# Kernel optimization log

Measured on AMD Instinct MI355X. Metric: run time of the kernel, lower is better.

## Reference

```python
import jax, jax.numpy as jnp
import numpy as np

N = 100000      # hits
K = 256         # max truth objects per event
C = 2           # n_ccoords
NCLS = 6        # n_classes
Q_MIN = 0.5
S_B = 1.0
ENERGY_DEN_OFFSET = 1.0
PAYLOAD_BETA_CLIP = 0.1
USE_AVG_CC = 0.0
BETA_CLIP = 1.0 - 1e-5


def _divide_no_nan(num, den):
    return jnp.where(den == 0.0, 0.0, num / jnp.where(den == 0.0, 1.0, den))


def setup_inputs() -> dict:
    key = jax.random.key(0)
    ks = jax.random.split(key, 12)
    pred_beta = jax.random.uniform(ks[0], (N, 1), minval=0.01, maxval=0.99)
    pred_ccoords = jax.random.normal(ks[1], (N, C))
    pred_energy = jax.random.uniform(ks[2], (N, 1), minval=0.0, maxval=100.0)
    pred_pos = 50.0 * jax.random.normal(ks[3], (N, 2))
    pred_time = jax.random.normal(ks[4], (N, 1))
    pred_id = jax.random.normal(ks[5], (N, NCLS))
    t_energy = jax.random.uniform(ks[6], (N, 1), minval=0.1, maxval=100.0)
    t_pos = 50.0 * jax.random.normal(ks[7], (N, 2))
    t_time = jax.random.normal(ks[8], (N, 1))
    t_pid = jax.random.randint(ks[9], (N, 1), 1, NCLS + 1).astype(jnp.float32)
    t_idx = jax.random.randint(ks[10], (N, 1), -1, K)  # -1 == noise
    rowsplits = jnp.array([0, N], dtype=jnp.int32)
    return dict(pred_beta=pred_beta, pred_ccoords=pred_ccoords,
                pred_energy=pred_energy, pred_pos=pred_pos,
                pred_time=pred_time, pred_id=pred_id,
                t_energy=t_energy, t_pos=t_pos, t_time=t_time, t_pid=t_pid,
                t_idx=t_idx, rowsplits=rowsplits)


def oc_loss(pred_beta, pred_ccoords, pred_energy, pred_pos, pred_time,
            pred_id, t_energy, t_pos, t_time, t_pid, t_idx):
    beta = jnp.clip(pred_beta[:, 0], 0.0, BETA_CLIP)          # [N]
    q = jnp.arctanh(beta) ** 2 + Q_MIN                        # [N] charge
    tidx = t_idx[:, 0]
    not_noise = tidx >= 0                                     # [N]
    tclip = jnp.where(not_noise, tidx, 0)

    # hit->object assignment matrix [N, K]
    M = jax.nn.one_hot(tclip, K, dtype=beta.dtype) * not_noise[:, None].astype(beta.dtype)
    counts = M.sum(axis=0)                                    # [K]
    obj_valid = counts > 0.0
    n_valid = jnp.maximum(obj_valid.sum().astype(beta.dtype), 1.0)

    # condensation point per object: highest-beta hit of that object
    score = jnp.where(M > 0.0, beta[:, None], -1.0)           # [N, K]
    alpha = jnp.argmax(score, axis=0)                         # [K]
    x_alpha = pred_ccoords[alpha]                             # [K, C]
    mean_cc = (M.T @ pred_ccoords) / jnp.maximum(counts, 1.0)[:, None]
    x_k = USE_AVG_CC * mean_cc + (1.0 - USE_AVG_CC) * x_alpha
    q_alpha = q[alpha]                                        # [K]
    beta_alpha = beta[alpha]

    # pairwise hit <-> condensation-point squared distances [N, K]
    diff = pred_ccoords[:, None, :] - x_k[None, :, :]
    distsq = jnp.sum(diff * diff, axis=-1)

    qq = q[:, None] * q_alpha[None, :]                        # [N, K]
    # attractive potential: own-object hits pulled toward condensation point
    v_att_k = (M * distsq * qq).sum(axis=0) / jnp.maximum(counts, 1.0)
    V_att = jnp.where(obj_valid, v_att_k, 0.0).sum() / n_valid
    # repulsive potential: all other hits pushed out of a unit ball
    hinge = jax.nn.relu(1.0 - jnp.sqrt(distsq + 1e-6))
    v_rep_k = ((1.0 - M) * hinge * qq).sum(axis=0) / jnp.maximum(N - counts, 1.0)
    V_rep = jnp.where(obj_valid, v_rep_k, 0.0).sum() / n_valid

    # beta terms: sharpen condensation points, suppress noise beta
    L_beta = jnp.where(obj_valid, 1.0 - beta_alpha, 0.0).sum() / n_valid
    n_noise = jnp.maximum((~not_noise).astype(beta.dtype).sum(), 1.0)
    L_noise = S_B * jnp.where(not_noise, 0.0, beta).sum() / n_noise

    # --- per-hit payload losses ---
    ew = jax.nn.relu(jnp.where(t_energy > 10.0,
                               1.0, (t_energy - 0.5) / 10.0 * 10.0 / 9.5))
    e_loss = _divide_no_nan((t_energy - pred_energy) ** 2,
                            t_energy + ENERGY_DEN_OFFSET)
    p_loss = jnp.sum((t_pos - pred_pos) ** 2, axis=-1, keepdims=True) / 100.0
    tm_loss = (t_time - pred_time) ** 2
    cls_loss = 1e-8 * jnp.mean(pred_id ** 2, axis=-1, keepdims=True)
    payload = jnp.concatenate([e_loss, p_loss, tm_loss, cls_loss], axis=-1) * ew  # [N,4]
    payload = jnp.where(pred_beta < PAYLOAD_BETA_CLIP, 0.0, payload)

    # beta-weighted average of payload over each truth object
    pw = beta * not_noise.astype(beta.dtype)                  # [N]
    num = M.T @ (payload * pw[:, None])                       # [K, 4]
    den = (M * pw[:, None]).sum(axis=0)                       # [K]
    per_obj = num / jnp.maximum(den, 1e-6)[:, None]
    L_payload = (jnp.where(obj_valid[:, None], per_obj, 0.0).sum(axis=0) / n_valid).sum()

    return V_att + V_rep + L_beta + L_noise + L_payload


def reference(pred_beta, pred_ccoords, pred_energy, pred_pos, pred_time,
              pred_id, t_energy, t_pos, t_time, t_pid, t_idx, rowsplits):
    return oc_loss(pred_beta, pred_ccoords, pred_energy, pred_pos, pred_time,
                   pred_id, t_energy, t_pos, t_time, t_pid, t_idx)
```

## Files before the change

kernel.cpp:

```cpp
#include <hip/hip_runtime.h>
#include <hip/hip_bf16.h>
#include <math.h>

#define KOBJ 256
#define B1   256
#define NBH  391
#define HSTR 392
#define QMIN 0.5f
#define BETA_CLIP_C (1.0f - 1e-5f)

typedef unsigned long long u64;

__global__ __launch_bounds__(256) void partials(
    const float*  __restrict__ pred_beta,
    const float*  __restrict__ pred_energy,
    const float2* __restrict__ pred_pos,
    const float*  __restrict__ pred_time,
    const float2* __restrict__ pred_id2,
    const float*  __restrict__ t_energy,
    const float2* __restrict__ t_pos,
    const float*  __restrict__ t_time,
    const int*    __restrict__ t_idx,
    u64*    __restrict__ pk_part,
    float*  __restrict__ cnt_part,
    float*  __restrict__ den_part,
    float4* __restrict__ num_part,
    float*  __restrict__ noise_part,
    int n)
{
    __shared__ u64   spk[KOBJ];
    __shared__ float scnt[KOBJ];
    __shared__ float sden[KOBJ], sn0[KOBJ], sn1[KOBJ], sn2[KOBJ], sn3[KOBJ];
    __shared__ float snoise[256];
    int t = threadIdx.x;
    int b = blockIdx.x;
    spk[t] = 0; scnt[t] = 0.f; sden[t] = 0.f;
    sn0[t] = 0.f; sn1[t] = 0.f; sn2[t] = 0.f; sn3[t] = 0.f;
    __syncthreads();

    float noise = 0.0f;
    for (int i = b * 256 + t; i < n; i += B1 * 256) {
        int tid = t_idx[i];
        float braw = pred_beta[i];
        float beta = fminf(fmaxf(braw, 0.0f), BETA_CLIP_C);
        if (tid >= 0) {
            atomicAdd(&scnt[tid], 1.0f);
            u64 key = ((u64)__float_as_uint(beta) << 32) |
                      (u64)(0x7FFFFFFFu - (unsigned)i);
            atomicMax(&spk[tid], key);
            float te = t_energy[i];
            float ew = (te > 10.0f) ? 1.0f : fmaxf(0.0f, (te - 0.5f) / 9.5f);
            float de = te - pred_energy[i];
            float el = de * de / (te + 1.0f);
            float2 tp = t_pos[i];
            float2 pp = pred_pos[i];
            float dpx = tp.x - pp.x, dpy = tp.y - pp.y;
            float pl = (dpx * dpx + dpy * dpy) * 0.01f;
            float dt = t_time[i] - pred_time[i];
            float tl = dt * dt;
            float2 id0 = pred_id2[3 * i];
            float2 id1 = pred_id2[3 * i + 1];
            float2 id2 = pred_id2[3 * i + 2];
            float cs = id0.x * id0.x + id0.y * id0.y + id1.x * id1.x +
                       id1.y * id1.y + id2.x * id2.x + id2.y * id2.y;
            cs *= (1e-8f / 6.0f);
            float mask = (braw < 0.1f) ? 0.0f : 1.0f;
            float w = mask * ew * beta;
            atomicAdd(&sden[tid], beta);
            atomicAdd(&sn0[tid], el * w);
            atomicAdd(&sn1[tid], pl * w);
            atomicAdd(&sn2[tid], tl * w);
            atomicAdd(&sn3[tid], cs * w);
        } else {
            noise += beta;
        }
    }
    __syncthreads();
    int o = t * B1 + b;
    pk_part[o]  = spk[t];
    cnt_part[o] = scnt[t];
    den_part[o] = sden[t];
    num_part[o] = make_float4(sn0[t], sn1[t], sn2[t], sn3[t]);
    snoise[t] = noise;
    __syncthreads();
    for (int s = 128; s > 0; s >>= 1) {
        if (t < s) snoise[t] += snoise[t + s];
        __syncthreads();
    }
    if (t == 0) noise_part[b] = snoise[0];
}

__global__ __launch_bounds__(256) void merge(
    const float2* __restrict__ pred_ccoords,
    const u64*    __restrict__ pk_part,
    const float*  __restrict__ cnt_part,
    const float*  __restrict__ den_part,
    const float4* __restrict__ num_part,
    float4* __restrict__ objA,
    float4* __restrict__ objB)
{
    __shared__ u64   spk[256];
    __shared__ float scnt[256], sden[256], snum[256];
    int k = blockIdx.x;
    int b = threadIdx.x;
    int o = k * B1 + b;
    u64 pk = pk_part[o];
    float cnt = cnt_part[o];
    float den = den_part[o];
    float4 v = num_part[o];
    float nsum = v.x + v.y + v.z + v.w;
    spk[b] = pk; scnt[b] = cnt; sden[b] = den; snum[b] = nsum;
    __syncthreads();
    for (int s = 128; s > 0; s >>= 1) {
        if (b < s) {
            u64 p = spk[b + s]; if (p > spk[b]) spk[b] = p;
            scnt[b] += scnt[b + s];
            sden[b] += sden[b + s];
            snum[b] += snum[b + s];
        }
        __syncthreads();
    }
    if (b == 0) {
        float cs = scnt[0];
        bool valid = cs > 0.f;
        float xk = 0.f, yk = 0.f, qa = 0.f, lb = 0.f, pay = 0.f;
        if (valid) {
            u64 p = spk[0];
            unsigned a = 0x7FFFFFFFu - (unsigned)(p & 0xFFFFFFFFull);
            float ba = __uint_as_float((unsigned)(p >> 32));
            float2 cc = pred_ccoords[a];
            xk = cc.x; yk = cc.y;
            float at = atanhf(ba);
            qa = at * at + QMIN;
            lb = 1.0f - ba;
            pay = snum[0] / fmaxf(sden[0], 1e-6f);
        }
        objA[k] = make_float4(xk, yk, qa, cs);
        objB[k] = make_float4(pay, lb, valid ? 1.f : 0.f, 0.f);
    }
}

__global__ __launch_bounds__(256) void heavy(
    const float*  __restrict__ pred_beta,
    const float2* __restrict__ pred_ccoords,
    const int*    __restrict__ t_idx,
    const float4* __restrict__ objA,
    float* __restrict__ rep_part,
    float* __restrict__ att_part,
    int n)
{
    __shared__ float4 pts[256];
    int t = threadIdx.x;
    int p = blockIdx.x * 256 + t;
    float4 pt;
    if (p < n) {
        float beta = fminf(fmaxf(pred_beta[p], 0.0f), BETA_CLIP_C);
        float at = atanhf(beta);
        float2 cc = pred_ccoords[p];
        pt = make_float4(cc.x, cc.y, at * at + QMIN, __int_as_float(t_idx[p]));
    } else {
        pt = make_float4(0.f, 0.f, 0.f, __int_as_float(-2));
    }
    pts[t] = pt;
    float4 oa = objA[t];
    float xk = oa.x, yk = oa.y;
    __syncthreads();
    float rep = 0.f, att = 0.f;
    #pragma unroll 8
    for (int j = 0; j < 256; ++j) {
        float4 s = pts[j];
        float dx = s.x - xk, dy = s.y - yk;
        float d2 = fmaf(dx, dx, dy * dy);
        float r = __builtin_amdgcn_sqrtf(d2 + 1e-6f);
        float h = fmaxf(0.0f, 1.0f - r);
        bool own = (__float_as_int(s.w) == t);
        rep = fmaf(own ? 0.0f : h,  s.z, rep);
        att = fmaf(own ? d2 : 0.0f, s.z, att);
    }
    int o = t * HSTR + blockIdx.x;
    rep_part[o] = rep;
    att_part[o] = att;
}

__global__ __launch_bounds__(256) void final1(
    const float4* __restrict__ objA,
    const float4* __restrict__ objB,
    const float*  __restrict__ rep_part,
    const float*  __restrict__ att_part,
    float4* __restrict__ objC,
    int n, int nbh)
{
    __shared__ float srep[256], satt[256];
    int k = blockIdx.x;
    int b = threadIdx.x;
    float rep = 0.f, att = 0.f;
    int o = k * HSTR + b;
    if (b < nbh)        { rep += rep_part[o];        att += att_part[o]; }
    if (b + 256 < nbh)  { rep += rep_part[o + 256];  att += att_part[o + 256]; }
    srep[b] = rep; satt[b] = att;
    __syncthreads();
    for (int s = 128; s > 0; s >>= 1) {
        if (b < s) { srep[b] += srep[b + s]; satt[b] += satt[b + s]; }
        __syncthreads();
    }
    if (b == 0) {
        float4 a  = objA[k];
        float4 b4 = objB[k];
        float cnt = a.w, qa = a.z, valid = b4.z;
        float vatt = valid * satt[0] * qa / fmaxf(cnt, 1.0f);
        float vrep = valid * srep[0] * qa / fmaxf((float)n - cnt, 1.0f);
        objC[k] = make_float4(vatt + vrep + b4.y + b4.x, valid, cnt, 0.f);
    }
}

__global__ __launch_bounds__(256) void final2(
    const float4* __restrict__ objC,
    const float*  __restrict__ noise_part,
    float* __restrict__ out, int n)
{
    __shared__ float4 sred[256];
    int t = threadIdx.x;
    float4 c = objC[t];
    c.w = noise_part[t];
    sred[t] = c;
    __syncthreads();
    for (int s = 128; s > 0; s >>= 1) {
        if (t < s) {
            float4 x = sred[t], y = sred[t + s];
            sred[t] = make_float4(x.x + y.x, x.y + y.y, x.z + y.z, x.w + y.w);
        }
        __syncthreads();
    }
    if (t == 0) {
        float4 r = sred[0];
        float nv = fmaxf(r.y, 1.0f);
        float nnoise = fmaxf((float)n - r.z, 1.0f);
        out[0] = r.x / nv + r.w / nnoise;
    }
}

extern "C" void kernel_launch(void* const* d_in, const int* in_sizes, int n_in,
                              void* d_out, int out_size, void* d_ws, size_t ws_size,
                              hipStream_t stream) {
    const float*  pred_beta    = (const float*)d_in[0];
    const float2* pred_ccoords = (const float2*)d_in[1];
    const float*  pred_energy  = (const float*)d_in[2];
    const float2* pred_pos     = (const float2*)d_in[3];
    const float*  pred_time    = (const float*)d_in[4];
    const float2* pred_id2     = (const float2*)d_in[5];
    const float*  t_energy     = (const float*)d_in[6];
    const float2* t_pos        = (const float2*)d_in[7];
    const float*  t_time       = (const float*)d_in[8];
    const int*    t_idx        = (const int*)d_in[10];
    int n = in_sizes[0];
    int nbh = (n + 255) / 256;

    char* base = (char*)d_ws;
    u64*    pk_part    = (u64*)   (base);
    float*  cnt_part   = (float*) (base + 524288);
    float*  den_part   = (float*) (base + 786432);
    float4* num_part   = (float4*)(base + 1048576);
    float*  noise_part = (float*) (base + 2097152);
    float4* objA       = (float4*)(base + 2098176);
    float4* objB       = (float4*)(base + 2102272);
    float4* objC       = (float4*)(base + 2106368);
    float*  rep_part   = (float*) (base + 2110464);
    float*  att_part   = (float*) (base + 2511872);

    partials<<<B1, 256, 0, stream>>>(pred_beta, pred_energy, pred_pos, pred_time,
                                     pred_id2, t_energy, t_pos, t_time, t_idx,
                                     pk_part, cnt_part, den_part, num_part, noise_part, n);
    merge<<<KOBJ, 256, 0, stream>>>(pred_ccoords, pk_part, cnt_part, den_part, num_part,
                                    objA, objB);
    heavy<<<nbh, 256, 0, stream>>>(pred_beta, pred_ccoords, t_idx, objA,
                                   rep_part, att_part, n);
    final1<<<KOBJ, 256, 0, stream>>>(objA, objB, rep_part, att_part, objC, n, nbh);
    final2<<<1, 256, 0, stream>>>(objC, noise_part, (float*)d_out, n);
}
```

Measured before the change: 108.1 us.

## Fuse merge and final kernels, precompute point records, cut partial blocks

The pipeline shrinks from five kernels to three. The partials kernel now also writes per-hit (x, y, q, tidx) records, and it runs on 64 blocks instead of 256. Each heavy block reduces the per-block max keys for its object itself, instead of relying on a separate merge kernel. The final kernel combines per-object reductions and finishes with a last-block atomic counter, which removes launch overhead and the final2 kernel. In exchange, the partials kernel has less parallelism, every heavy block redundantly reduces 64 keys per object, and the heavy kernel reads points from global memory instead of shared memory.

```diff
diff --git a/kernel.cpp b/kernel.cpp
--- a/kernel.cpp
+++ b/kernel.cpp
@@ -3,16 +3,16 @@
 #include <math.h>
 
 #define KOBJ 256
-#define B1   256
-#define NBH  391
-#define HSTR 392
+#define B1   64
 #define QMIN 0.5f
 #define BETA_CLIP_C (1.0f - 1e-5f)
 
 typedef unsigned long long u64;
 
+
 __global__ __launch_bounds__(256) void partials(
     const float*  __restrict__ pred_beta,
+    const float2* __restrict__ pred_ccoords,
     const float*  __restrict__ pred_energy,
     const float2* __restrict__ pred_pos,
     const float*  __restrict__ pred_time,
@@ -21,12 +21,15 @@
     const float2* __restrict__ t_pos,
     const float*  __restrict__ t_time,
     const int*    __restrict__ t_idx,
-    u64*    __restrict__ pk_part,
-    float*  __restrict__ cnt_part,
-    float*  __restrict__ den_part,
-    float4* __restrict__ num_part,
+    float4* __restrict__ pts4,
+    u64*    __restrict__ pkb,
+    u64*    __restrict__ pkk,
+    float*  __restrict__ cntk,
+    float*  __restrict__ denk,
+    float4* __restrict__ numk,
     float*  __restrict__ noise_part,
-    int n)
+    float*  __restrict__ accum,
+    int n, int npad)
 {
     __shared__ u64   spk[KOBJ];
     __shared__ float scnt[KOBJ];
@@ -36,51 +39,59 @@
     int b = blockIdx.x;
     spk[t] = 0; scnt[t] = 0.f; sden[t] = 0.f;
     sn0[t] = 0.f; sn1[t] = 0.f; sn2[t] = 0.f; sn3[t] = 0.f;
+    if (b == 0 && t < 8) accum[t] = 0.0f;
     __syncthreads();
 
     float noise = 0.0f;
-    for (int i = b * 256 + t; i < n; i += B1 * 256) {
-        int tid = t_idx[i];
-        float braw = pred_beta[i];
-        float beta = fminf(fmaxf(braw, 0.0f), BETA_CLIP_C);
-        if (tid >= 0) {
-            atomicAdd(&scnt[tid], 1.0f);
-            u64 key = ((u64)__float_as_uint(beta) << 32) |
-                      (u64)(0x7FFFFFFFu - (unsigned)i);
-            atomicMax(&spk[tid], key);
-            float te = t_energy[i];
-            float ew = (te > 10.0f) ? 1.0f : fmaxf(0.0f, (te - 0.5f) / 9.5f);
-            float de = te - pred_energy[i];
-            float el = de * de / (te + 1.0f);
-            float2 tp = t_pos[i];
-            float2 pp = pred_pos[i];
-            float dpx = tp.x - pp.x, dpy = tp.y - pp.y;
-            float pl = (dpx * dpx + dpy * dpy) * 0.01f;
-            float dt = t_time[i] - pred_time[i];
-            float tl = dt * dt;
-            float2 id0 = pred_id2[3 * i];
-            float2 id1 = pred_id2[3 * i + 1];
-            float2 id2 = pred_id2[3 * i + 2];
-            float cs = id0.x * id0.x + id0.y * id0.y + id1.x * id1.x +
-                       id1.y * id1.y + id2.x * id2.x + id2.y * id2.y;
-            cs *= (1e-8f / 6.0f);
-            float mask = (braw < 0.1f) ? 0.0f : 1.0f;
-            float w = mask * ew * beta;
-            atomicAdd(&sden[tid], beta);
-            atomicAdd(&sn0[tid], el * w);
-            atomicAdd(&sn1[tid], pl * w);
-            atomicAdd(&sn2[tid], tl * w);
-            atomicAdd(&sn3[tid], cs * w);
+    for (int i = b * 256 + t; i < npad; i += B1 * 256) {
+        if (i < n) {
+            int tid = t_idx[i];
+            float braw = pred_beta[i];
+            float beta = fminf(fmaxf(braw, 0.0f), BETA_CLIP_C);
+            float at = atanhf(beta);
+            float2 cc = pred_ccoords[i];
+            pts4[i] = make_float4(cc.x, cc.y, at * at + QMIN, __int_as_float(tid));
+            if (tid >= 0) {
+                atomicAdd(&scnt[tid], 1.0f);
+                u64 key = ((u64)__float_as_uint(beta) << 32) |
+                          (u64)(0x7FFFFFFFu - (unsigned)i);
+                atomicMax(&spk[tid], key);
+                float te = t_energy[i];
+                float ew = (te > 10.0f) ? 1.0f : fmaxf(0.0f, (te - 0.5f) / 9.5f);
+                float de = te - pred_energy[i];
+                float el = de * de / (te + 1.0f);
+                float2 tp = t_pos[i];
+                float2 pp = pred_pos[i];
+                float dpx = tp.x - pp.x, dpy = tp.y - pp.y;
+                float pl = (dpx * dpx + dpy * dpy) * 0.01f;
+                float dt = t_time[i] - pred_time[i];
+                float tl = dt * dt;
+                float2 id0 = pred_id2[3 * i];
+                float2 id1 = pred_id2[3 * i + 1];
+                float2 id2 = pred_id2[3 * i + 2];
+                float cs = id0.x * id0.x + id0.y * id0.y + id1.x * id1.x +
+                           id1.y * id1.y + id2.x * id2.x + id2.y * id2.y;
+                cs *= (1e-8f / 6.0f);
+                float mask = (braw < 0.1f) ? 0.0f : 1.0f;
+                float w = mask * ew * beta;
+                atomicAdd(&sden[tid], beta);
+                atomicAdd(&sn0[tid], el * w);
+                atomicAdd(&sn1[tid], pl * w);
+                atomicAdd(&sn2[tid], tl * w);
+                atomicAdd(&sn3[tid], cs * w);
+            } else {
+                noise += beta;
+            }
         } else {
-            noise += beta;
-        }
-    }
-    __syncthreads();
-    int o = t * B1 + b;
-    pk_part[o]  = spk[t];
-    cnt_part[o] = scnt[t];
-    den_part[o] = sden[t];
-    num_part[o] = make_float4(sn0[t], sn1[t], sn2[t], sn3[t]);
+            pts4[i] = make_float4(0.f, 0.f, 0.f, __int_as_float(-2));
+        }
+    }
+    __syncthreads();
+    pkb[b * KOBJ + t] = spk[t];
+    pkk[t * B1 + b]   = spk[t];
+    cntk[t * B1 + b]  = scnt[t];
+    denk[t * B1 + b]  = sden[t];
+    numk[t * B1 + b]  = make_float4(sn0[t], sn1[t], sn2[t], sn3[t]);
     snoise[t] = noise;
     __syncthreads();
     for (int s = 128; s > 0; s >>= 1) {
@@ -90,85 +101,32 @@
     if (t == 0) noise_part[b] = snoise[0];
 }
 
-__global__ __launch_bounds__(256) void merge(
+__global__ __launch_bounds__(256) void heavy(
     const float2* __restrict__ pred_ccoords,
-    const u64*    __restrict__ pk_part,
-    const float*  __restrict__ cnt_part,
-    const float*  __restrict__ den_part,
-    const float4* __restrict__ num_part,
-    float4* __restrict__ objA,
-    float4* __restrict__ objB)
-{
-    __shared__ u64   spk[256];
-    __shared__ float scnt[256], sden[256], snum[256];
-    int k = blockIdx.x;
-    int b = threadIdx.x;
-    int o = k * B1 + b;
-    u64 pk = pk_part[o];
-    float cnt = cnt_part[o];
-    float den = den_part[o];
-    float4 v = num_part[o];
-    float nsum = v.x + v.y + v.z + v.w;
-    spk[b] = pk; scnt[b] = cnt; sden[b] = den; snum[b] = nsum;
-    __syncthreads();
-    for (int s = 128; s > 0; s >>= 1) {
-        if (b < s) {
-            u64 p = spk[b + s]; if (p > spk[b]) spk[b] = p;
-            scnt[b] += scnt[b + s];
-            sden[b] += sden[b + s];
-            snum[b] += snum[b + s];
-        }
-        __syncthreads();
-    }
-    if (b == 0) {
-        float cs = scnt[0];
-        bool valid = cs > 0.f;
-        float xk = 0.f, yk = 0.f, qa = 0.f, lb = 0.f, pay = 0.f;
-        if (valid) {
-            u64 p = spk[0];
-            unsigned a = 0x7FFFFFFFu - (unsigned)(p & 0xFFFFFFFFull);
-            float ba = __uint_as_float((unsigned)(p >> 32));
-            float2 cc = pred_ccoords[a];
-            xk = cc.x; yk = cc.y;
-            float at = atanhf(ba);
-            qa = at * at + QMIN;
-            lb = 1.0f - ba;
-            pay = snum[0] / fmaxf(sden[0], 1e-6f);
-        }
-        objA[k] = make_float4(xk, yk, qa, cs);
-        objB[k] = make_float4(pay, lb, valid ? 1.f : 0.f, 0.f);
-    }
-}
-
-__global__ __launch_bounds__(256) void heavy(
-    const float*  __restrict__ pred_beta,
-    const float2* __restrict__ pred_ccoords,
-    const int*    __restrict__ t_idx,
-    const float4* __restrict__ objA,
+    const u64*    __restrict__ pkb,
+    const float4* __restrict__ pts4,
     float* __restrict__ rep_part,
     float* __restrict__ att_part,
-    int n)
+    int hstr)
 {
-    __shared__ float4 pts[256];
     int t = threadIdx.x;
-    int p = blockIdx.x * 256 + t;
-    float4 pt;
-    if (p < n) {
-        float beta = fminf(fmaxf(pred_beta[p], 0.0f), BETA_CLIP_C);
-        float at = atanhf(beta);
-        float2 cc = pred_ccoords[p];
-        pt = make_float4(cc.x, cc.y, at * at + QMIN, __int_as_float(t_idx[p]));
-    } else {
-        pt = make_float4(0.f, 0.f, 0.f, __int_as_float(-2));
-    }
-    pts[t] = pt;
-    float4 oa = objA[t];
-    float xk = oa.x, yk = oa.y;
-    __syncthreads();
+    u64 pk = 0;
+    #pragma unroll 8
+    for (int b = 0; b < B1; ++b) {
+        u64 p = pkb[b * KOBJ + t];
+        pk = (p > pk) ? p : pk;
+    }
+    float xk = 0.f, yk = 0.f;
+    if (pk != 0) {
+        unsigned a = 0x7FFFFFFFu - (unsigned)(pk & 0xFFFFFFFFull);
+        float2 cc = pred_ccoords[a];
+        xk = cc.x; yk = cc.y;
+    }
+    const float4* __restrict__ chunk = pts4 + (size_t)blockIdx.x * 256;
     float rep = 0.f, att = 0.f;
     #pragma unroll 8
     for (int j = 0; j < 256; ++j) {
-        float4 s = pts[j];
+        float4 s = chunk[j];
         float dx = s.x - xk, dy = s.y - yk;
         float d2 = fmaf(dx, dx, dy * dy);
         float r = __builtin_amdgcn_sqrtf(d2 + 1e-6f);
@@ -177,65 +135,82 @@
         rep = fmaf(own ? 0.0f : h,  s.z, rep);
         att = fmaf(own ? d2 : 0.0f, s.z, att);
     }
-    int o = t * HSTR + blockIdx.x;
+    int o = t * hstr + blockIdx.x;
     rep_part[o] = rep;
     att_part[o] = att;
 }
 
-__global__ __launch_bounds__(256) void final1(
-    const float4* __restrict__ objA,
-    const float4* __restrict__ objB,
+__global__ __launch_bounds__(256) void final_k(
+    const u64*    __restrict__ pkk,
+    const float*  __restrict__ cntk,
+    const float*  __restrict__ denk,
+    const float4* __restrict__ numk,
     const float*  __restrict__ rep_part,
     const float*  __restrict__ att_part,
-    float4* __restrict__ objC,
-    int n, int nbh)
+    const float*  __restrict__ noise_part,
+    float* __restrict__ accum,
+    float* __restrict__ out,
+    int n, int nbh, int hstr)
 {
-    __shared__ float srep[256], satt[256];
+    __shared__ float srep[256], satt[256], scnt[256], sden[256], snum[256], snoi[256];
+    __shared__ u64 spk[256];
     int k = blockIdx.x;
-    int b = threadIdx.x;
+    int t = threadIdx.x;
     float rep = 0.f, att = 0.f;
-    int o = k * HSTR + b;
-    if (b < nbh)        { rep += rep_part[o];        att += att_part[o]; }
-    if (b + 256 < nbh)  { rep += rep_part[o + 256];  att += att_part[o + 256]; }
-    srep[b] = rep; satt[b] = att;
-    __syncthreads();
-    for (int s = 128; s > 0; s >>= 1) {
-        if (b < s) { srep[b] += srep[b + s]; satt[b] += satt[b + s]; }
-        __syncthreads();
-    }
-    if (b == 0) {
-        float4 a  = objA[k];
-        float4 b4 = objB[k];
-        float cnt = a.w, qa = a.z, valid = b4.z;
-        float vatt = valid * satt[0] * qa / fmaxf(cnt, 1.0f);
-        float vrep = valid * srep[0] * qa / fmaxf((float)n - cnt, 1.0f);
-        objC[k] = make_float4(vatt + vrep + b4.y + b4.x, valid, cnt, 0.f);
-    }
-}
-
-__global__ __launch_bounds__(256) void final2(
-    const float4* __restrict__ objC,
-    const float*  __restrict__ noise_part,
-    float* __restrict__ out, int n)
-{
-    __shared__ float4 sred[256];
-    int t = threadIdx.x;
-    float4 c = objC[t];
-    c.w = noise_part[t];
-    sred[t] = c;
+    int o = k * hstr + t;
+    if (t < nbh)        { rep += rep_part[o];        att += att_part[o]; }
+    if (t + 256 < nbh)  { rep += rep_part[o + 256];  att += att_part[o + 256]; }
+    u64 pk = 0; float cnt = 0.f, den = 0.f, ns = 0.f, noi = 0.f;
+    if (t < B1) {
+        int p = k * B1 + t;
+        pk = pkk[p];
+        cnt = cntk[p];
+        den = denk[p];
+        float4 v = numk[p];
+        ns = v.x + v.y + v.z + v.w;
+        if (k == 0) noi = noise_part[t];
+    }
+    srep[t] = rep; satt[t] = att; scnt[t] = cnt; sden[t] = den;
+    snum[t] = ns; snoi[t] = noi; spk[t] = pk;
     __syncthreads();
     for (int s = 128; s > 0; s >>= 1) {
         if (t < s) {
-            float4 x = sred[t], y = sred[t + s];
-            sred[t] = make_float4(x.x + y.x, x.y + y.y, x.z + y.z, x.w + y.w);
+            srep[t] += srep[t + s]; satt[t] += satt[t + s];
+            scnt[t] += scnt[t + s]; sden[t] += sden[t + s];
+            snum[t] += snum[t + s]; snoi[t] += snoi[t + s];
+            u64 p = spk[t + s]; if (p > spk[t]) spk[t] = p;
         }
         __syncthreads();
     }
     if (t == 0) {
-        float4 r = sred[0];
-        float nv = fmaxf(r.y, 1.0f);
-        float nnoise = fmaxf((float)n - r.z, 1.0f);
-        out[0] = r.x / nv + r.w / nnoise;
+        u64 p = spk[0];
+        float cs = scnt[0];
+        float s0 = 0.f, valid = 0.f;
+        if (p != 0) {
+            valid = 1.f;
+            float ba = __uint_as_float((unsigned)(p >> 32));
+            float at = atanhf(ba);
+            float qa = at * at + QMIN;
+            float lb = 1.0f - ba;
+            float pay = snum[0] / fmaxf(sden[0], 1e-6f);
+            float vatt = satt[0] * qa / fmaxf(cs, 1.0f);
+            float vrep = srep[0] * qa / fmaxf((float)n - cs, 1.0f);
+            s0 = vatt + vrep + lb + pay;
+        }
+        atomicAdd(&accum[0], s0);
+        atomicAdd(&accum[1], valid);
+        atomicAdd(&accum[2], cs);
+        atomicAdd(&accum[3], snoi[0]);
+        __threadfence();
+        int prev = atomicAdd((int*)&accum[4], 1);
+        if (prev == KOBJ - 1) {
+            __threadfence();
+            volatile float* va = accum;
+            float ssum = va[0], nvs = va[1], csum = va[2], nsum = va[3];
+            float nv = fmaxf(nvs, 1.0f);
+            float nnoise = fmaxf((float)n - csum, 1.0f);
+            out[0] = ssum / nv + nsum / nnoise;
+        }
     }
 }
 
@@ -254,26 +229,27 @@
     const int*    t_idx        = (const int*)d_in[10];
     int n = in_sizes[0];
     int nbh = (n + 255) / 256;
+    int npad = nbh * 256;
+    int hstr = (nbh + 8) & ~7;
 
     char* base = (char*)d_ws;
-    u64*    pk_part    = (u64*)   (base);
-    float*  cnt_part   = (float*) (base + 524288);
-    float*  den_part   = (float*) (base + 786432);
-    float4* num_part   = (float4*)(base + 1048576);
-    float*  noise_part = (float*) (base + 2097152);
-    float4* objA       = (float4*)(base + 2098176);
-    float4* objB       = (float4*)(base + 2102272);
-    float4* objC       = (float4*)(base + 2106368);
-    float*  rep_part   = (float*) (base + 2110464);
-    float*  att_part   = (float*) (base + 2511872);
-
-    partials<<<B1, 256, 0, stream>>>(pred_beta, pred_energy, pred_pos, pred_time,
-                                     pred_id2, t_energy, t_pos, t_time, t_idx,
-                                     pk_part, cnt_part, den_part, num_part, noise_part, n);
-    merge<<<KOBJ, 256, 0, stream>>>(pred_ccoords, pk_part, cnt_part, den_part, num_part,
-                                    objA, objB);
-    heavy<<<nbh, 256, 0, stream>>>(pred_beta, pred_ccoords, t_idx, objA,
-                                   rep_part, att_part, n);
-    final1<<<KOBJ, 256, 0, stream>>>(objA, objB, rep_part, att_part, objC, n, nbh);
-    final2<<<1, 256, 0, stream>>>(objC, noise_part, (float*)d_out, n);
-}
+    size_t off = 0;
+    float4* pts4  = (float4*)(base + off); off += (size_t)npad * 16;
+    u64*    pkb   = (u64*)   (base + off); off += (size_t)B1 * KOBJ * 8;
+    u64*    pkk   = (u64*)   (base + off); off += (size_t)KOBJ * B1 * 8;
+    float*  cntk  = (float*) (base + off); off += (size_t)KOBJ * B1 * 4;
+    float*  denk  = (float*) (base + off); off += (size_t)KOBJ * B1 * 4;
+    float4* numk  = (float4*)(base + off); off += (size_t)KOBJ * B1 * 16;
+    float*  noise_part = (float*)(base + off); off += 256 * 4;
+    float*  accum = (float*) (base + off); off += 64;
+    float*  rep_part = (float*)(base + off); off += (size_t)KOBJ * hstr * 4;
+    float*  att_part = (float*)(base + off); off += (size_t)KOBJ * hstr * 4;
+
+    partials<<<B1, 256, 0, stream>>>(pred_beta, pred_ccoords, pred_energy, pred_pos,
+                                     pred_time, pred_id2, t_energy, t_pos, t_time, t_idx,
+                                     pts4, pkb, pkk, cntk, denk, numk, noise_part, accum,
+                                     n, npad);
+    heavy<<<nbh, 256, 0, stream>>>(pred_ccoords, pkb, pts4, rep_part, att_part, hstr);
+    final_k<<<KOBJ, 256, 0, stream>>>(pkk, cntk, denk, numk, rep_part, att_part,
+                                      noise_part, accum, (float*)d_out, n, nbh, hstr);
+}
```

Result: slower. 137.3 us (+27.0%).

## Register-block four objects per thread in heavy kernel, split hits across waves

Applied to the files above, without the earlier changes.

Each wave in the heavy kernel now handles a quarter of the block's hits, and each lane keeps four objects in registers. This amortizes every LDS read of a hit over four objects, cutting shared-memory traffic per distance computation. Per-wave partials are combined through shared memory and written as float4 per object per block, and final1 sums those float4 components. The cost is a larger partial buffer (four times the bytes), more registers, and an extra reduction step plus a barrier.

```diff
diff --git a/kernel.cpp b/kernel.cpp
--- a/kernel.cpp
+++ b/kernel.cpp
@@ -4,8 +4,6 @@
 
 #define KOBJ 256
 #define B1   256
-#define NBH  391
-#define HSTR 392
 #define QMIN 0.5f
 #define BETA_CLIP_C (1.0f - 1e-5f)
 
@@ -145,12 +143,14 @@
     const float2* __restrict__ pred_ccoords,
     const int*    __restrict__ t_idx,
     const float4* __restrict__ objA,
-    float* __restrict__ rep_part,
-    float* __restrict__ att_part,
-    int n)
+    float4* __restrict__ rep4,
+    float4* __restrict__ att4,
+    int n, int hstr)
 {
     __shared__ float4 pts[256];
+    __shared__ float sred[2][4][256];
     int t = threadIdx.x;
+    int l = t & 63, w = t >> 6;
     int p = blockIdx.x * 256 + t;
     float4 pt;
     if (p < n) {
@@ -162,41 +162,61 @@
         pt = make_float4(0.f, 0.f, 0.f, __int_as_float(-2));
     }
     pts[t] = pt;
-    float4 oa = objA[t];
-    float xk = oa.x, yk = oa.y;
-    __syncthreads();
-    float rep = 0.f, att = 0.f;
-    #pragma unroll 8
-    for (int j = 0; j < 256; ++j) {
-        float4 s = pts[j];
-        float dx = s.x - xk, dy = s.y - yk;
-        float d2 = fmaf(dx, dx, dy * dy);
-        float r = __builtin_amdgcn_sqrtf(d2 + 1e-6f);
-        float h = fmaxf(0.0f, 1.0f - r);
-        bool own = (__float_as_int(s.w) == t);
-        rep = fmaf(own ? 0.0f : h,  s.z, rep);
-        att = fmaf(own ? d2 : 0.0f, s.z, att);
-    }
-    int o = t * HSTR + blockIdx.x;
-    rep_part[o] = rep;
-    att_part[o] = att;
+    float xk[4], yk[4];
+    #pragma unroll
+    for (int ki = 0; ki < 4; ++ki) {
+        float4 oa = objA[ki * 64 + l];
+        xk[ki] = oa.x; yk[ki] = oa.y;
+    }
+    __syncthreads();
+    float rep[4] = {0.f, 0.f, 0.f, 0.f};
+    float att[4] = {0.f, 0.f, 0.f, 0.f};
+    const int base = w * 64;
+    #pragma unroll 4
+    for (int j = 0; j < 64; ++j) {
+        float4 s = pts[base + j];
+        #pragma unroll
+        for (int ki = 0; ki < 4; ++ki) {
+            float dx = s.x - xk[ki], dy = s.y - yk[ki];
+            float d2 = fmaf(dx, dx, dy * dy);
+            float r = __builtin_amdgcn_sqrtf(d2 + 1e-6f);
+            float h = fmaxf(0.0f, 1.0f - r);
+            bool own = (__float_as_int(s.w) == ki * 64 + l);
+            rep[ki] = fmaf(own ? 0.0f : h,  s.z, rep[ki]);
+            att[ki] = fmaf(own ? d2 : 0.0f, s.z, att[ki]);
+        }
+    }
+    #pragma unroll
+    for (int ki = 0; ki < 4; ++ki) {
+        sred[0][w][ki * 64 + l] = rep[ki];
+        sred[1][w][ki * 64 + l] = att[ki];
+    }
+    __syncthreads();
+    float4 r4 = make_float4(sred[0][0][t], sred[0][1][t], sred[0][2][t], sred[0][3][t]);
+    float4 a4 = make_float4(sred[1][0][t], sred[1][1][t], sred[1][2][t], sred[1][3][t]);
+    int o = t * hstr + blockIdx.x;
+    rep4[o] = r4;
+    att4[o] = a4;
 }
 
 __global__ __launch_bounds__(256) void final1(
     const float4* __restrict__ objA,
     const float4* __restrict__ objB,
-    const float*  __restrict__ rep_part,
-    const float*  __restrict__ att_part,
+    const float4* __restrict__ rep4,
+    const float4* __restrict__ att4,
     float4* __restrict__ objC,
-    int n, int nbh)
+    int n, int nbh, int hstr)
 {
     __shared__ float srep[256], satt[256];
     int k = blockIdx.x;
     int b = threadIdx.x;
     float rep = 0.f, att = 0.f;
-    int o = k * HSTR + b;
-    if (b < nbh)        { rep += rep_part[o];        att += att_part[o]; }
-    if (b + 256 < nbh)  { rep += rep_part[o + 256];  att += att_part[o + 256]; }
+    for (int c = b; c < nbh; c += 256) {
+        float4 r = rep4[k * hstr + c];
+        float4 a = att4[k * hstr + c];
+        rep += r.x + r.y + r.z + r.w;
+        att += a.x + a.y + a.z + a.w;
+    }
     srep[b] = rep; satt[b] = att;
     __syncthreads();
     for (int s = 128; s > 0; s >>= 1) {
@@ -254,18 +274,20 @@
     const int*    t_idx        = (const int*)d_in[10];
     int n = in_sizes[0];
     int nbh = (n + 255) / 256;
+    int hstr = (nbh + 8) & ~7;
 
     char* base = (char*)d_ws;
-    u64*    pk_part    = (u64*)   (base);
-    float*  cnt_part   = (float*) (base + 524288);
-    float*  den_part   = (float*) (base + 786432);
-    float4* num_part   = (float4*)(base + 1048576);
-    float*  noise_part = (float*) (base + 2097152);
-    float4* objA       = (float4*)(base + 2098176);
-    float4* objB       = (float4*)(base + 2102272);
-    float4* objC       = (float4*)(base + 2106368);
-    float*  rep_part   = (float*) (base + 2110464);
-    float*  att_part   = (float*) (base + 2511872);
+    size_t off = 0;
+    u64*    pk_part    = (u64*)   (base + off); off += (size_t)KOBJ * B1 * 8;
+    float*  cnt_part   = (float*) (base + off); off += (size_t)KOBJ * B1 * 4;
+    float*  den_part   = (float*) (base + off); off += (size_t)KOBJ * B1 * 4;
+    float4* num_part   = (float4*)(base + off); off += (size_t)KOBJ * B1 * 16;
+    float*  noise_part = (float*) (base + off); off += 256 * 4;
+    float4* objA       = (float4*)(base + off); off += KOBJ * 16;
+    float4* objB       = (float4*)(base + off); off += KOBJ * 16;
+    float4* objC       = (float4*)(base + off); off += KOBJ * 16;
+    float4* rep4       = (float4*)(base + off); off += (size_t)KOBJ * hstr * 16;
+    float4* att4       = (float4*)(base + off); off += (size_t)KOBJ * hstr * 16;
 
     partials<<<B1, 256, 0, stream>>>(pred_beta, pred_energy, pred_pos, pred_time,
                                      pred_id2, t_energy, t_pos, t_time, t_idx,
@@ -273,7 +295,7 @@
     merge<<<KOBJ, 256, 0, stream>>>(pred_ccoords, pk_part, cnt_part, den_part, num_part,
                                     objA, objB);
     heavy<<<nbh, 256, 0, stream>>>(pred_beta, pred_ccoords, t_idx, objA,
-                                   rep_part, att_part, n);
-    final1<<<KOBJ, 256, 0, stream>>>(objA, objB, rep_part, att_part, objC, n, nbh);
+                                   rep4, att4, n, hstr);
+    final1<<<KOBJ, 256, 0, stream>>>(objA, objB, rep4, att4, objC, n, nbh, hstr);
     final2<<<1, 256, 0, stream>>>(objC, noise_part, (float*)d_out, n);
 }
```

Result: slower. 110.7 us (+2.4%).
